# Optimization experiments

Measured on AMD Instinct MI355X. Metric: run time of the kernel, lower is better.

## Reference

```python
import jax, jax.numpy as jnp
import numpy as np

# Fixed tetrahedral (kanchor=4) rotation->anchor permutation table, taken verbatim
# from the docstring in the original source (trace_idx_ori).
TRACE_IDX_ORI = jnp.array([
    [0, 1, 2, 3], [0, 2, 3, 1], [0, 3, 1, 2],
    [1, 2, 0, 3], [1, 0, 3, 2], [1, 3, 2, 0],
    [2, 3, 0, 1], [2, 0, 1, 3], [2, 1, 3, 0],
    [3, 1, 0, 2], [3, 0, 2, 1], [3, 2, 1, 0]], dtype=jnp.int32)

B, A, N, M, D, H = 1, 4, 384, 384, 256, 8
C = D // H  # d_model_per_head = 32
NR = TRACE_IDX_ORI.shape[0]  # 12 rotations


def _project_heads(x, W, b):
    # x: (b, a, n, d) -> (b, a, h, n, c)
    y = x @ W.T + b
    bb, aa, nn, _ = y.shape
    return y.reshape(bb, aa, nn, H, C).transpose(0, 1, 3, 2, 4)


def setup_inputs() -> dict:
    key = jax.random.key(0)
    ks = jax.random.split(key, 6)
    s = 1.0 / np.sqrt(D).astype(np.float32)
    return {
        "input_q": jax.random.normal(ks[0], (B, A, N, D), dtype=jnp.float32),
        "input_k": jax.random.normal(ks[1], (B, A, M, D), dtype=jnp.float32),
        "input_v": jax.random.normal(ks[2], (B, A, M, D), dtype=jnp.float32),
        "Wq": jax.random.normal(ks[3], (D, D), dtype=jnp.float32) * s,
        "bq": jnp.zeros((D,), dtype=jnp.float32),
        "Wk": jax.random.normal(ks[4], (D, D), dtype=jnp.float32) * s,
        "bk": jnp.zeros((D,), dtype=jnp.float32),
        "Wv": jax.random.normal(ks[5], (D, D), dtype=jnp.float32) * s,
        "bv": jnp.zeros((D,), dtype=jnp.float32),
    }


def reference(input_q, input_k, input_v, Wq, bq, Wk, bk, Wv, bv):
    # Step 0: linear projections + split heads.  q,k,v: (b, a, h, n|m, c)
    q = _project_heads(input_q, Wq, bq)
    k = _project_heads(input_k, Wk, bk)
    v = _project_heads(input_v, Wv, bv)

    # Step 1: per-anchor-pair local attention scores: (b, a, e, h, n, m)
    scores_ae = jnp.einsum('bahnc,behmc->baehnm', q, k) / jnp.sqrt(
        jnp.asarray(C, dtype=q.dtype))

    # Step 2: rotation-wise gather (attn_mode='r_soft', alternative_impl=False).
    # For rotation r, query anchor a attends to key anchor trace_idx_ori[r, a]:
    # scores_rot[b, r, a] = scores_ae[b, a, trace_idx_ori[r, a]]  -> (b, nr, a, h, n, m)
    a_idx = jnp.arange(A, dtype=jnp.int32)[None, :]  # (1, A) broadcasts vs (NR, A)
    scores_rot = scores_ae[:, a_idx, TRACE_IDX_ORI]

    # Global rotation attention: pool over anchors/heads/points (attn_r_summ='mean',
    # attn_r_multihead=False), make non-negative ('sq'), normalize over rotations.
    pooled = jnp.mean(scores_rot, axis=(2, 3, 4, 5))  # (b, nr)
    pos = pooled * pooled
    attn_r = pos / jnp.sum(pos, axis=-1, keepdims=True)  # (b, nr)

    # Step 3+4: softmax over key points per rotation, gather values per rotation,
    # then weight by the global rotation attention.
    attn_local = jax.nn.softmax(scores_rot, axis=-1)  # (b, nr, a, h, n, m)
    v_rot = v[:, TRACE_IDX_ORI]  # (b, nr, a, h, m, c)
    hidden = jnp.einsum('br,brahnm,brahmc->bahnc', attn_r, attn_local, v_rot)

    # Merge heads: (b, a, h, n, c) -> (b, a, n, h*c)
    out = hidden.transpose(0, 1, 3, 2, 4).reshape(B, A, N, D)
    return out
```

## Files before the change

### kernel.cpp

```cpp
#include <hip/hip_runtime.h>
#include <hip/hip_bf16.h>

typedef __attribute__((ext_vector_type(8))) short s8x8;
typedef __attribute__((ext_vector_type(4))) float f32x4;

union FragU { s8x8 v; unsigned d[4]; };

__device__ __forceinline__ ushort f2bf(float x) {
    union { float f; unsigned u; } c; c.f = x;
    unsigned r = c.u + 0x7FFFu + ((c.u >> 16) & 1u);
    return (ushort)(r >> 16);
}
__device__ __forceinline__ float bf2f(ushort b) {
    union { unsigned u; float f; } c; c.u = ((unsigned)b) << 16;
    return c.f;
}
__device__ __forceinline__ unsigned cvt_pk(float lo, float hi) {
    unsigned r;
    asm("v_cvt_pk_bf16_f32 %0, %1, %2" : "=v"(r) : "v"(lo), "v"(hi));
    return r;
}
__device__ __forceinline__ float asf(unsigned u) {
    union { unsigned u; float f; } c; c.u = u; return c.f;
}

__global__ __launch_bounds__(64) void proj_kernel(
    const float* __restrict__ Xq, const float* __restrict__ Xk,
    const float* __restrict__ Xv,
    const float* __restrict__ Wq, const float* __restrict__ bq,
    const float* __restrict__ Wk, const float* __restrict__ bk,
    const float* __restrict__ Wv, const float* __restrict__ bv,
    ushort* __restrict__ qh, ushort* __restrict__ ql,
    ushort* __restrict__ kh, ushort* __restrict__ kl,
    ushort* __restrict__ vh, float* __restrict__ part)
{
    const int z = blockIdx.z;
    const float* X    = (z == 0) ? Xq : (z == 1) ? Xk : Xv;
    const float* W    = (z == 0) ? Wq : (z == 1) ? Wk : Wv;
    const float* bias = (z == 0) ? bq : (z == 1) ? bk : bv;

    const int lane = threadIdx.x;
    const int lg   = lane >> 4;
    const int ll   = lane & 15;
    const int bx   = blockIdx.x;
    const int row0 = bx * 16;
    const int col0 = blockIdx.y * 64;

    f32x4 acc[4];
    #pragma unroll
    for (int ct = 0; ct < 4; ++ct) acc[ct] = (f32x4){0.f, 0.f, 0.f, 0.f};

    for (int kk = 0; kk < 8; ++kk) {
        FragU ah, al;
        {
            const float* xp = &X[(size_t)(row0 + ll) * 256 + kk * 32 + lg * 8];
            const float4 x0 = *(const float4*)&xp[0];
            const float4 x1 = *(const float4*)&xp[4];
            const float xv[8] = {x0.x, x0.y, x0.z, x0.w, x1.x, x1.y, x1.z, x1.w};
            #pragma unroll
            for (int i = 0; i < 4; ++i) {
                const unsigned hd = cvt_pk(xv[2 * i], xv[2 * i + 1]);
                ah.d[i] = hd;
                al.d[i] = cvt_pk(xv[2 * i]     - asf(hd << 16),
                                 xv[2 * i + 1] - asf(hd & 0xffff0000u));
            }
        }
        #pragma unroll
        for (int ct = 0; ct < 4; ++ct) {
            const float* wp = &W[(size_t)(col0 + ct * 16 + ll) * 256 + kk * 32 + lg * 8];
            const float4 w0 = *(const float4*)&wp[0];
            const float4 w1 = *(const float4*)&wp[4];
            const float wv[8] = {w0.x, w0.y, w0.z, w0.w, w1.x, w1.y, w1.z, w1.w};
            FragU bh, bl;
            #pragma unroll
            for (int i = 0; i < 4; ++i) {
                const unsigned hd = cvt_pk(wv[2 * i], wv[2 * i + 1]);
                bh.d[i] = hd;
                bl.d[i] = cvt_pk(wv[2 * i]     - asf(hd << 16),
                                 wv[2 * i + 1] - asf(hd & 0xffff0000u));
            }
            acc[ct] = __builtin_amdgcn_mfma_f32_16x16x32_bf16(ah.v, bh.v, acc[ct], 0, 0, 0);
            acc[ct] = __builtin_amdgcn_mfma_f32_16x16x32_bf16(al.v, bh.v, acc[ct], 0, 0, 0);
            acc[ct] = __builtin_amdgcn_mfma_f32_16x16x32_bf16(ah.v, bl.v, acc[ct], 0, 0, 0);
        }
    }

    const int ae  = bx / 24;
    const int rbl = bx - ae * 24;
    float bct[4];
    #pragma unroll
    for (int ct = 0; ct < 4; ++ct) bct[ct] = bias[col0 + ct * 16 + ll];

    if (z != 2) {
        #pragma unroll
        for (int ct = 0; ct < 4; ++ct) {
            const int d = col0 + ct * 16 + ll;
            const int hd = d >> 5;
            const int c = d & 31;
            #pragma unroll
            for (int j = 0; j < 4; ++j) {
                const int n = rbl * 16 + lg * 4 + j;
                const float v = acc[ct][j] + bct[ct];
                const ushort hb = f2bf(v);
                const ushort lb = f2bf(v - bf2f(hb));
                if (z == 0) {
                    const size_t idx = ((size_t)((ae * 8 + hd) * 384 + n)) * 32 + c;
                    qh[idx] = hb; ql[idx] = lb;
                } else {
                    const size_t idx =
                        ((size_t)(((ae * 8 + hd) * 4 + (c >> 3)) * 384 + n)) * 8 + (c & 7);
                    kh[idx] = hb; kl[idx] = lb;
                }
            }
        }
        #pragma unroll
        for (int ct = 0; ct < 4; ++ct) {
            float cs = 4.f * bct[ct];
            #pragma unroll
            for (int j = 0; j < 4; ++j) cs += acc[ct][j];
            cs += __shfl_xor(cs, 16);
            cs += __shfl_xor(cs, 32);
            if (lg == 0)
                part[((size_t)(z * 4 + ae) * 24 + rbl) * 256 + col0 + ct * 16 + ll] = cs;
        }
    } else {
        #pragma unroll
        for (int ct = 0; ct < 4; ++ct) {
            const int d = col0 + ct * 16 + ll;
            const int hd = d >> 5;
            const int c = d & 31;
            ushort p[4];
            #pragma unroll
            for (int j = 0; j < 4; ++j) p[j] = f2bf(acc[ct][j] + bct[ct]);
            const int m0 = rbl * 16 + lg * 4;
            const size_t basei = ((size_t)((ae * 8 + hd) * 32 + c)) * 384 + m0;
            *(uint2*)&vh[basei] =
                make_uint2((unsigned)p[0] | ((unsigned)p[1] << 16),
                           (unsigned)p[2] | ((unsigned)p[3] << 16));
        }
    }
}

__global__ __launch_bounds__(256) void stats_kernel(
    const float* __restrict__ part, float* __restrict__ wout)
{
    __shared__ float ws4[4][16];
    __shared__ float cellsh[16];
    const int tid = threadIdx.x;
    const int lane = tid & 63;
    const int wv = tid >> 6;

    float qs[4], ks[4];
    #pragma unroll
    for (int a2 = 0; a2 < 4; ++a2) {
        const float* pq = &part[(size_t)(0 * 4 + a2) * 24 * 256 + tid];
        const float* pk = &part[(size_t)(1 * 4 + a2) * 24 * 256 + tid];
        float sq = 0.f, sk = 0.f;
        #pragma unroll
        for (int r = 0; r < 24; ++r) {
            sq += pq[r * 256];
            sk += pk[r * 256];
        }
        qs[a2] = sq; ks[a2] = sk;
    }
    #pragma unroll
    for (int i = 0; i < 16; ++i) {
        float v = qs[i >> 2] * ks[i & 3];
        v += __shfl_xor(v, 1);
        v += __shfl_xor(v, 2);
        v += __shfl_xor(v, 4);
        v += __shfl_xor(v, 8);
        v += __shfl_xor(v, 16);
        v += __shfl_xor(v, 32);
        if (lane == 0) ws4[wv][i] = v;
    }
    __syncthreads();
    if (tid < 16)
        cellsh[tid] = 0.17677669529663687f *
            (ws4[0][tid] + ws4[1][tid] + ws4[2][tid] + ws4[3][tid]);
    __syncthreads();
    if (tid == 0) {
        const int TR[12][4] = {
            {0,1,2,3},{0,2,3,1},{0,3,1,2},{1,2,0,3},{1,0,3,2},{1,3,2,0},
            {2,3,0,1},{2,0,1,3},{2,1,3,0},{3,1,0,2},{3,0,2,1},{3,2,1,0}};
        const float denom = 4.0f * 8.0f * 384.0f * 384.0f;
        float pos[12];
        float psum = 0.f;
        for (int r = 0; r < 12; ++r) {
            float s = 0.f;
            for (int a2 = 0; a2 < 4; ++a2) s += cellsh[a2 * 4 + TR[r][a2]];
            const float pooled = s / denom;
            pos[r] = pooled * pooled;
            psum += pos[r];
        }
        float w[16];
        for (int i = 0; i < 16; ++i) w[i] = 0.f;
        const float ip = 1.f / psum;
        for (int r = 0; r < 12; ++r)
            for (int a2 = 0; a2 < 4; ++a2) w[a2 * 4 + TR[r][a2]] += pos[r] * ip;
        for (int i = 0; i < 16; ++i) wout[i] = w[i];
    }
}

__global__ __launch_bounds__(192) void attn_mfma_kernel(
    const ushort* __restrict__ qhb, const ushort* __restrict__ qlb,
    const ushort* __restrict__ khb, const ushort* __restrict__ klb,
    const ushort* __restrict__ vhb, float* __restrict__ Sout)
{
    __shared__ ushort Kh[4 * 1544];
    __shared__ ushort Kl[4 * 1544];
    __shared__ ushort Vh[32 * 200];
    __shared__ ushort Pl[3 * 2 * 16 * 40];

    const int strip = blockIdx.x;
    const int aeh   = blockIdx.y;
    const int hh    = aeh & 7;
    const int ee    = (aeh >> 3) & 3;
    const int aa    = aeh >> 5;
    const int e8h   = ee * 8 + hh;
    const int a8h   = aa * 8 + hh;
    const int tid   = threadIdx.x;
    const int wave  = tid >> 6;
    const int lane  = tid & 63;
    const int lg    = lane >> 4;
    const int ll    = lane & 15;

    s8x8 qfh[2], qfl[2];
    #pragma unroll
    for (int r = 0; r < 2; ++r) {
        const int n0 = strip * 96 + (2 * wave + r) * 16;
        const size_t off = (size_t)(a8h * 384 + n0 + ll) * 32 + lg * 8;
        qfh[r] = *(const s8x8*)&qhb[off];
        qfl[r] = *(const s8x8*)&qlb[off];
    }

    f32x4 oacc[2][2];
    #pragma unroll
    for (int r = 0; r < 2; ++r)
        #pragma unroll
        for (int ct = 0; ct < 2; ++ct)
            oacc[r][ct] = (f32x4){0.f, 0.f, 0.f, 0.f};
    float lsum[2][4];
    #pragma unroll
    for (int r = 0; r < 2; ++r)
        #pragma unroll
        for (int j = 0; j < 4; ++j) lsum[r][j] = 0.f;
    const float sc = 0.17677669529663687f;

    for (int half = 0; half < 2; ++half) {
        #pragma unroll
        for (int i = 0; i < 4; ++i) {
            const size_t src = ((size_t)(e8h * 4 + i) * 384 + half * 192 + tid) * 8;
            *(uint4*)&Kh[i * 1544 + tid * 8] = *(const uint4*)&khb[src];
            *(uint4*)&Kl[i * 1544 + tid * 8] = *(const uint4*)&klb[src];
        }
        #pragma unroll
        for (int i = 0; i < 4; ++i) {
            const int u = tid + 192 * i;
            const int c = u / 24;
            const int m8 = (u - c * 24) * 8;
            *(uint4*)&Vh[c * 200 + m8] =
                *(const uint4*)&vhb[(size_t)(e8h * 32 + c) * 384 + half * 192 + m8];
        }
        __syncthreads();

        for (int mt2 = 0; mt2 < 6; ++mt2) {
            #pragma unroll
            for (int sub = 0; sub < 2; ++sub) {
                const int mt = mt2 * 2 + sub;
                const s8x8 kfh = *(const s8x8*)&Kh[lg * 1544 + (mt * 16 + ll) * 8];
                const s8x8 kfl = *(const s8x8*)&Kl[lg * 1544 + (mt * 16 + ll) * 8];
                #pragma unroll
                for (int r = 0; r < 2; ++r) {
                    f32x4 s = {0.f, 0.f, 0.f, 0.f};
                    __builtin_amdgcn_s_setprio(1);
                    s = __builtin_amdgcn_mfma_f32_16x16x32_bf16(qfh[r], kfh, s, 0, 0, 0);
                    s = __builtin_amdgcn_mfma_f32_16x16x32_bf16(qfl[r], kfh, s, 0, 0, 0);
                    s = __builtin_amdgcn_mfma_f32_16x16x32_bf16(qfh[r], kfl, s, 0, 0, 0);
                    __builtin_amdgcn_s_setprio(0);
                    #pragma unroll
                    for (int j = 0; j < 4; ++j) {
                        const float p = __expf(s[j] * sc);
                        lsum[r][j] += p;
                        Pl[((wave * 2 + r) * 16 + lg * 4 + j) * 40 + sub * 16 + ll] = f2bf(p);
                    }
                }
            }
            const int mloc = mt2 * 32;
            const s8x8 vf0 = *(const s8x8*)&Vh[(0  + ll) * 200 + mloc + lg * 8];
            const s8x8 vf1 = *(const s8x8*)&Vh[(16 + ll) * 200 + mloc + lg * 8];
            #pragma unroll
            for (int r = 0; r < 2; ++r) {
                const s8x8 pa = *(const s8x8*)&Pl[((wave * 2 + r) * 16 + ll) * 40 + lg * 8];
                __builtin_amdgcn_s_setprio(1);
                oacc[r][0] = __builtin_amdgcn_mfma_f32_16x16x32_bf16(pa, vf0, oacc[r][0], 0, 0, 0);
                oacc[r][1] = __builtin_amdgcn_mfma_f32_16x16x32_bf16(pa, vf1, oacc[r][1], 0, 0, 0);
                __builtin_amdgcn_s_setprio(0);
            }
        }
        __syncthreads();
    }

    #pragma unroll
    for (int r = 0; r < 2; ++r) {
        #pragma unroll
        for (int j = 0; j < 4; ++j) {
            float L = lsum[r][j];
            L += __shfl_xor(L, 1);
            L += __shfl_xor(L, 2);
            L += __shfl_xor(L, 4);
            L += __shfl_xor(L, 8);
            const float invL = 1.f / L;
            const int row = strip * 96 + (2 * wave + r) * 16 + lg * 4 + j;
            const size_t base = (size_t)(aeh * 384 + row) * 32;
            Sout[base + 0  + ll] = oacc[r][0][j] * invL;
            Sout[base + 16 + ll] = oacc[r][1][j] * invL;
        }
    }
}

__global__ __launch_bounds__(256) void combine_kernel(
    const float* __restrict__ S, const float* __restrict__ wbuf,
    float* __restrict__ out)
{
    __shared__ float wsh[16];
    const int tid = threadIdx.x;
    if (tid < 16) wsh[tid] = wbuf[tid];
    __syncthreads();

    const int idx4 = blockIdx.x * 256 + tid;
    const int a = idx4 / 24576;
    const int rem = idx4 - a * 24576;
    const int n = rem >> 6;
    const int d4 = rem & 63;
    const int h = d4 >> 3;
    const int c0 = (d4 & 7) * 4;
    float4 r = make_float4(0.f, 0.f, 0.f, 0.f);
    #pragma unroll
    for (int e = 0; e < 4; ++e) {
        const float wv2 = wsh[a * 4 + e];
        const float4 s = *(const float4*)&S[(size_t)(((a * 4 + e) * 8 + h) * 384 + n) * 32 + c0];
        r.x += wv2 * s.x; r.y += wv2 * s.y; r.z += wv2 * s.z; r.w += wv2 * s.w;
    }
    *(float4*)&out[(size_t)idx4 * 4] = r;
}

extern "C" void kernel_launch(void* const* d_in, const int* in_sizes, int n_in,
                              void* d_out, int out_size, void* d_ws, size_t ws_size,
                              hipStream_t stream)
{
    const float* in_q = (const float*)d_in[0];
    const float* in_k = (const float*)d_in[1];
    const float* in_v = (const float*)d_in[2];
    const float* Wq   = (const float*)d_in[3];
    const float* bq   = (const float*)d_in[4];
    const float* Wk   = (const float*)d_in[5];
    const float* bk   = (const float*)d_in[6];
    const float* Wv   = (const float*)d_in[7];
    const float* bv   = (const float*)d_in[8];

    ushort* qh = (ushort*)d_ws;
    ushort* ql = qh + 393216;
    ushort* kh = ql + 393216;
    ushort* kl = kh + 393216;
    ushort* vh = kl + 393216;
    float*  Sb = (float*)(vh + 393216);
    float*  pt = Sb + 1572864;
    float*  wb = pt + 49152;
    float*  outp = (float*)d_out;

    dim3 pgrid(96, 4, 3);
    proj_kernel<<<pgrid, 64, 0, stream>>>(in_q, in_k, in_v, Wq, bq, Wk, bk,
                                          Wv, bv, qh, ql, kh, kl, vh, pt);
    stats_kernel<<<1, 256, 0, stream>>>(pt, wb);
    dim3 agrid(4, 128);
    attn_mfma_kernel<<<agrid, 192, 0, stream>>>(qh, ql, kh, kl, vh, Sb);
    combine_kernel<<<384, 256, 0, stream>>>(Sb, wb, outp);
}
```

Before: 47.31 us.

## Fuse rotation-weighted combine into attention kernel, loop over key anchors in-block

The attention kernel now owns one (anchor, head) pair and a 48-row query strip, and loops over all four key anchors inside the block. It weights each anchor's normalized output by the rotation weight and accumulates in registers, then writes the final merged-head output directly. This removes the fp32 intermediate buffer S and the separate combine kernel launch, along with their global write and read traffic. In exchange each wave holds one query tile instead of two, so K/V shared-memory tiles get less reuse per load. The grid is also smaller (256 blocks instead of 512), with a longer serial loop per block.

```diff
diff --git a/kernel.cpp b/kernel.cpp
--- a/kernel.cpp
+++ b/kernel.cpp
@@ -202,147 +202,116 @@
     }
 }
 
-__global__ __launch_bounds__(192) void attn_mfma_kernel(
+__global__ __launch_bounds__(192) void attn_fused_kernel(
     const ushort* __restrict__ qhb, const ushort* __restrict__ qlb,
     const ushort* __restrict__ khb, const ushort* __restrict__ klb,
-    const ushort* __restrict__ vhb, float* __restrict__ Sout)
+    const ushort* __restrict__ vhb, const float* __restrict__ wbuf,
+    float* __restrict__ out)
 {
     __shared__ ushort Kh[4 * 1544];
     __shared__ ushort Kl[4 * 1544];
     __shared__ ushort Vh[32 * 200];
-    __shared__ ushort Pl[3 * 2 * 16 * 40];
+    __shared__ ushort Pl[48 * 40];
 
     const int strip = blockIdx.x;
-    const int aeh   = blockIdx.y;
-    const int hh    = aeh & 7;
-    const int ee    = (aeh >> 3) & 3;
-    const int aa    = aeh >> 5;
-    const int e8h   = ee * 8 + hh;
-    const int a8h   = aa * 8 + hh;
+    const int ah    = blockIdx.y;
+    const int hh    = ah & 7;
+    const int aa    = ah >> 3;
     const int tid   = threadIdx.x;
     const int wave  = tid >> 6;
     const int lane  = tid & 63;
     const int lg    = lane >> 4;
     const int ll    = lane & 15;
 
-    s8x8 qfh[2], qfl[2];
-    #pragma unroll
-    for (int r = 0; r < 2; ++r) {
-        const int n0 = strip * 96 + (2 * wave + r) * 16;
-        const size_t off = (size_t)(a8h * 384 + n0 + ll) * 32 + lg * 8;
-        qfh[r] = *(const s8x8*)&qhb[off];
-        qfl[r] = *(const s8x8*)&qlb[off];
-    }
-
-    f32x4 oacc[2][2];
-    #pragma unroll
-    for (int r = 0; r < 2; ++r)
-        #pragma unroll
-        for (int ct = 0; ct < 2; ++ct)
-            oacc[r][ct] = (f32x4){0.f, 0.f, 0.f, 0.f};
-    float lsum[2][4];
-    #pragma unroll
-    for (int r = 0; r < 2; ++r)
-        #pragma unroll
-        for (int j = 0; j < 4; ++j) lsum[r][j] = 0.f;
+    const int n0 = strip * 48 + wave * 16;
+    s8x8 qfh, qfl;
+    {
+        const size_t off = (size_t)(ah * 384 + n0 + ll) * 32 + lg * 8;
+        qfh = *(const s8x8*)&qhb[off];
+        qfl = *(const s8x8*)&qlb[off];
+    }
+
+    f32x4 oout[2];
+    oout[0] = (f32x4){0.f, 0.f, 0.f, 0.f};
+    oout[1] = (f32x4){0.f, 0.f, 0.f, 0.f};
     const float sc = 0.17677669529663687f;
 
-    for (int half = 0; half < 2; ++half) {
-        #pragma unroll
-        for (int i = 0; i < 4; ++i) {
-            const size_t src = ((size_t)(e8h * 4 + i) * 384 + half * 192 + tid) * 8;
-            *(uint4*)&Kh[i * 1544 + tid * 8] = *(const uint4*)&khb[src];
-            *(uint4*)&Kl[i * 1544 + tid * 8] = *(const uint4*)&klb[src];
-        }
-        #pragma unroll
-        for (int i = 0; i < 4; ++i) {
-            const int u = tid + 192 * i;
-            const int c = u / 24;
-            const int m8 = (u - c * 24) * 8;
-            *(uint4*)&Vh[c * 200 + m8] =
-                *(const uint4*)&vhb[(size_t)(e8h * 32 + c) * 384 + half * 192 + m8];
-        }
-        __syncthreads();
-
-        for (int mt2 = 0; mt2 < 6; ++mt2) {
-            #pragma unroll
-            for (int sub = 0; sub < 2; ++sub) {
-                const int mt = mt2 * 2 + sub;
-                const s8x8 kfh = *(const s8x8*)&Kh[lg * 1544 + (mt * 16 + ll) * 8];
-                const s8x8 kfl = *(const s8x8*)&Kl[lg * 1544 + (mt * 16 + ll) * 8];
+    for (int e = 0; e < 4; ++e) {
+        const int e8h = e * 8 + hh;
+        f32x4 oacc[2];
+        oacc[0] = (f32x4){0.f, 0.f, 0.f, 0.f};
+        oacc[1] = (f32x4){0.f, 0.f, 0.f, 0.f};
+        float lsum[4] = {0.f, 0.f, 0.f, 0.f};
+
+        for (int half = 0; half < 2; ++half) {
+            #pragma unroll
+            for (int i = 0; i < 4; ++i) {
+                const size_t src = ((size_t)(e8h * 4 + i) * 384 + half * 192 + tid) * 8;
+                *(uint4*)&Kh[i * 1544 + tid * 8] = *(const uint4*)&khb[src];
+                *(uint4*)&Kl[i * 1544 + tid * 8] = *(const uint4*)&klb[src];
+            }
+            #pragma unroll
+            for (int i = 0; i < 4; ++i) {
+                const int u = tid + 192 * i;
+                const int c = u / 24;
+                const int m8 = (u - c * 24) * 8;
+                *(uint4*)&Vh[c * 200 + m8] =
+                    *(const uint4*)&vhb[(size_t)(e8h * 32 + c) * 384 + half * 192 + m8];
+            }
+            __syncthreads();
+
+            for (int mt2 = 0; mt2 < 6; ++mt2) {
                 #pragma unroll
-                for (int r = 0; r < 2; ++r) {
+                for (int sub = 0; sub < 2; ++sub) {
+                    const int mt = mt2 * 2 + sub;
+                    const s8x8 kfh = *(const s8x8*)&Kh[lg * 1544 + (mt * 16 + ll) * 8];
+                    const s8x8 kfl = *(const s8x8*)&Kl[lg * 1544 + (mt * 16 + ll) * 8];
                     f32x4 s = {0.f, 0.f, 0.f, 0.f};
                     __builtin_amdgcn_s_setprio(1);
-                    s = __builtin_amdgcn_mfma_f32_16x16x32_bf16(qfh[r], kfh, s, 0, 0, 0);
-                    s = __builtin_amdgcn_mfma_f32_16x16x32_bf16(qfl[r], kfh, s, 0, 0, 0);
-                    s = __builtin_amdgcn_mfma_f32_16x16x32_bf16(qfh[r], kfl, s, 0, 0, 0);
+                    s = __builtin_amdgcn_mfma_f32_16x16x32_bf16(qfh, kfh, s, 0, 0, 0);
+                    s = __builtin_amdgcn_mfma_f32_16x16x32_bf16(qfl, kfh, s, 0, 0, 0);
+                    s = __builtin_amdgcn_mfma_f32_16x16x32_bf16(qfh, kfl, s, 0, 0, 0);
                     __builtin_amdgcn_s_setprio(0);
                     #pragma unroll
                     for (int j = 0; j < 4; ++j) {
                         const float p = __expf(s[j] * sc);
-                        lsum[r][j] += p;
-                        Pl[((wave * 2 + r) * 16 + lg * 4 + j) * 40 + sub * 16 + ll] = f2bf(p);
+                        lsum[j] += p;
+                        Pl[(wave * 16 + lg * 4 + j) * 40 + sub * 16 + ll] = f2bf(p);
                     }
                 }
-            }
-            const int mloc = mt2 * 32;
-            const s8x8 vf0 = *(const s8x8*)&Vh[(0  + ll) * 200 + mloc + lg * 8];
-            const s8x8 vf1 = *(const s8x8*)&Vh[(16 + ll) * 200 + mloc + lg * 8];
-            #pragma unroll
-            for (int r = 0; r < 2; ++r) {
-                const s8x8 pa = *(const s8x8*)&Pl[((wave * 2 + r) * 16 + ll) * 40 + lg * 8];
+                const int mloc = mt2 * 32;
+                const s8x8 vf0 = *(const s8x8*)&Vh[(0  + ll) * 200 + mloc + lg * 8];
+                const s8x8 vf1 = *(const s8x8*)&Vh[(16 + ll) * 200 + mloc + lg * 8];
+                const s8x8 pa = *(const s8x8*)&Pl[(wave * 16 + ll) * 40 + lg * 8];
                 __builtin_amdgcn_s_setprio(1);
-                oacc[r][0] = __builtin_amdgcn_mfma_f32_16x16x32_bf16(pa, vf0, oacc[r][0], 0, 0, 0);
-                oacc[r][1] = __builtin_amdgcn_mfma_f32_16x16x32_bf16(pa, vf1, oacc[r][1], 0, 0, 0);
+                oacc[0] = __builtin_amdgcn_mfma_f32_16x16x32_bf16(pa, vf0, oacc[0], 0, 0, 0);
+                oacc[1] = __builtin_amdgcn_mfma_f32_16x16x32_bf16(pa, vf1, oacc[1], 0, 0, 0);
                 __builtin_amdgcn_s_setprio(0);
             }
-        }
-        __syncthreads();
-    }
-
-    #pragma unroll
-    for (int r = 0; r < 2; ++r) {
+            __syncthreads();
+        }
+
+        const float we = wbuf[aa * 4 + e];
         #pragma unroll
         for (int j = 0; j < 4; ++j) {
-            float L = lsum[r][j];
+            float L = lsum[j];
             L += __shfl_xor(L, 1);
             L += __shfl_xor(L, 2);
             L += __shfl_xor(L, 4);
             L += __shfl_xor(L, 8);
-            const float invL = 1.f / L;
-            const int row = strip * 96 + (2 * wave + r) * 16 + lg * 4 + j;
-            const size_t base = (size_t)(aeh * 384 + row) * 32;
-            Sout[base + 0  + ll] = oacc[r][0][j] * invL;
-            Sout[base + 16 + ll] = oacc[r][1][j] * invL;
-        }
-    }
-}
-
-__global__ __launch_bounds__(256) void combine_kernel(
-    const float* __restrict__ S, const float* __restrict__ wbuf,
-    float* __restrict__ out)
-{
-    __shared__ float wsh[16];
-    const int tid = threadIdx.x;
-    if (tid < 16) wsh[tid] = wbuf[tid];
-    __syncthreads();
-
-    const int idx4 = blockIdx.x * 256 + tid;
-    const int a = idx4 / 24576;
-    const int rem = idx4 - a * 24576;
-    const int n = rem >> 6;
-    const int d4 = rem & 63;
-    const int h = d4 >> 3;
-    const int c0 = (d4 & 7) * 4;
-    float4 r = make_float4(0.f, 0.f, 0.f, 0.f);
-    #pragma unroll
-    for (int e = 0; e < 4; ++e) {
-        const float wv2 = wsh[a * 4 + e];
-        const float4 s = *(const float4*)&S[(size_t)(((a * 4 + e) * 8 + h) * 384 + n) * 32 + c0];
-        r.x += wv2 * s.x; r.y += wv2 * s.y; r.z += wv2 * s.z; r.w += wv2 * s.w;
-    }
-    *(float4*)&out[(size_t)idx4 * 4] = r;
+            const float f = we / L;
+            oout[0][j] += f * oacc[0][j];
+            oout[1][j] += f * oacc[1][j];
+        }
+    }
+
+    #pragma unroll
+    for (int j = 0; j < 4; ++j) {
+        const int row = n0 + lg * 4 + j;
+        const size_t base = ((size_t)(aa * 384 + row)) * 256 + hh * 32;
+        out[base + 0  + ll] = oout[0][j];
+        out[base + 16 + ll] = oout[1][j];
+    }
 }
 
 extern "C" void kernel_launch(void* const* d_in, const int* in_sizes, int n_in,
@@ -364,8 +333,7 @@
     ushort* kh = ql + 393216;
     ushort* kl = kh + 393216;
     ushort* vh = kl + 393216;
-    float*  Sb = (float*)(vh + 393216);
-    float*  pt = Sb + 1572864;
+    float*  pt = (float*)(vh + 393216);
     float*  wb = pt + 49152;
     float*  outp = (float*)d_out;
 
@@ -373,7 +341,6 @@
     proj_kernel<<<pgrid, 64, 0, stream>>>(in_q, in_k, in_v, Wq, bq, Wk, bk,
                                           Wv, bv, qh, ql, kh, kl, vh, pt);
     stats_kernel<<<1, 256, 0, stream>>>(pt, wb);
-    dim3 agrid(4, 128);
-    attn_mfma_kernel<<<agrid, 192, 0, stream>>>(qh, ql, kh, kl, vh, Sb);
-    combine_kernel<<<384, 256, 0, stream>>>(Sb, wb, outp);
-}
+    dim3 agrid(8, 32);
+    attn_fused_kernel<<<agrid, 192, 0, stream>>>(qh, ql, kh, kl, vh, wb, outp);
+}
```

New measurement: 53.97 us. 14.1% more time.

## Keep softmax probabilities in registers via transposed QK MFMA; pack projection waves

Applied to the files above, without the earlier changes.

The attention kernel swaps the QK^T MFMA operand order so each lane holds score values that already match the A-operand layout of the PV MFMA. The probabilities are packed to bf16 in registers instead of going through a shared-memory round trip, and the V tile is stored to LDS with a permuted column order to match. The row-sum reduction changes from per-element sums with a 4-step shuffle to per-lane accumulation followed by cross-group shuffles and a broadcast. Separately, the projection kernel now packs three 64-thread tasks into each 192-thread block, cutting the block count.

```diff
diff --git a/kernel.cpp b/kernel.cpp
--- a/kernel.cpp
+++ b/kernel.cpp
@@ -24,7 +24,7 @@
     union { unsigned u; float f; } c; c.u = u; return c.f;
 }
 
-__global__ __launch_bounds__(64) void proj_kernel(
+__global__ __launch_bounds__(192) void proj_kernel(
     const float* __restrict__ Xq, const float* __restrict__ Xk,
     const float* __restrict__ Xv,
     const float* __restrict__ Wq, const float* __restrict__ bq,
@@ -34,17 +34,23 @@
     ushort* __restrict__ kh, ushort* __restrict__ kl,
     ushort* __restrict__ vh, float* __restrict__ part)
 {
-    const int z = blockIdx.z;
+    const int tid  = threadIdx.x;
+    const int wave = tid >> 6;
+    const int lane = tid & 63;
+    const int task = blockIdx.x * 3 + wave;
+    const int z    = task / 384;
+    const int rem  = task - z * 384;
+    const int by   = rem / 96;
+    const int bx   = rem - by * 96;
+
     const float* X    = (z == 0) ? Xq : (z == 1) ? Xk : Xv;
     const float* W    = (z == 0) ? Wq : (z == 1) ? Wk : Wv;
     const float* bias = (z == 0) ? bq : (z == 1) ? bk : bv;
 
-    const int lane = threadIdx.x;
     const int lg   = lane >> 4;
     const int ll   = lane & 15;
-    const int bx   = blockIdx.x;
     const int row0 = bx * 16;
-    const int col0 = blockIdx.y * 64;
+    const int col0 = by * 64;
 
     f32x4 acc[4];
     #pragma unroll
@@ -210,7 +216,6 @@
     __shared__ ushort Kh[4 * 1544];
     __shared__ ushort Kl[4 * 1544];
     __shared__ ushort Vh[32 * 200];
-    __shared__ ushort Pl[3 * 2 * 16 * 40];
 
     const int strip = blockIdx.x;
     const int aeh   = blockIdx.y;
@@ -240,11 +245,7 @@
         #pragma unroll
         for (int ct = 0; ct < 2; ++ct)
             oacc[r][ct] = (f32x4){0.f, 0.f, 0.f, 0.f};
-    float lsum[2][4];
-    #pragma unroll
-    for (int r = 0; r < 2; ++r)
-        #pragma unroll
-        for (int j = 0; j < 4; ++j) lsum[r][j] = 0.f;
+    float lsum[2] = {0.f, 0.f};
     const float sc = 0.17677669529663687f;
 
     for (int half = 0; half < 2; ++half) {
@@ -258,13 +259,19 @@
         for (int i = 0; i < 4; ++i) {
             const int u = tid + 192 * i;
             const int c = u / 24;
-            const int m8 = (u - c * 24) * 8;
-            *(uint4*)&Vh[c * 200 + m8] =
-                *(const uint4*)&vhb[(size_t)(e8h * 32 + c) * 384 + half * 192 + m8];
+            const int t = u - c * 24;
+            const int M = (t >> 2) * 32;
+            const int q2 = t & 3;
+            const int off = (q2 & 1) * 16 + (q2 >> 1) * 4;
+            const uint4 src = *(const uint4*)
+                &vhb[(size_t)(e8h * 32 + c) * 384 + half * 192 + t * 8];
+            *(uint2*)&Vh[c * 200 + M + off]     = make_uint2(src.x, src.y);
+            *(uint2*)&Vh[c * 200 + M + off + 8] = make_uint2(src.z, src.w);
         }
         __syncthreads();
 
         for (int mt2 = 0; mt2 < 6; ++mt2) {
+            float pv_[2][8];
             #pragma unroll
             for (int sub = 0; sub < 2; ++sub) {
                 const int mt = mt2 * 2 + sub;
@@ -274,15 +281,15 @@
                 for (int r = 0; r < 2; ++r) {
                     f32x4 s = {0.f, 0.f, 0.f, 0.f};
                     __builtin_amdgcn_s_setprio(1);
-                    s = __builtin_amdgcn_mfma_f32_16x16x32_bf16(qfh[r], kfh, s, 0, 0, 0);
-                    s = __builtin_amdgcn_mfma_f32_16x16x32_bf16(qfl[r], kfh, s, 0, 0, 0);
-                    s = __builtin_amdgcn_mfma_f32_16x16x32_bf16(qfh[r], kfl, s, 0, 0, 0);
+                    s = __builtin_amdgcn_mfma_f32_16x16x32_bf16(kfh, qfh[r], s, 0, 0, 0);
+                    s = __builtin_amdgcn_mfma_f32_16x16x32_bf16(kfl, qfh[r], s, 0, 0, 0);
+                    s = __builtin_amdgcn_mfma_f32_16x16x32_bf16(kfh, qfl[r], s, 0, 0, 0);
                     __builtin_amdgcn_s_setprio(0);
                     #pragma unroll
                     for (int j = 0; j < 4; ++j) {
                         const float p = __expf(s[j] * sc);
-                        lsum[r][j] += p;
-                        Pl[((wave * 2 + r) * 16 + lg * 4 + j) * 40 + sub * 16 + ll] = f2bf(p);
+                        lsum[r] += p;
+                        pv_[r][sub * 4 + j] = p;
                     }
                 }
             }
@@ -291,10 +298,14 @@
             const s8x8 vf1 = *(const s8x8*)&Vh[(16 + ll) * 200 + mloc + lg * 8];
             #pragma unroll
             for (int r = 0; r < 2; ++r) {
-                const s8x8 pa = *(const s8x8*)&Pl[((wave * 2 + r) * 16 + ll) * 40 + lg * 8];
+                FragU pu;
+                pu.d[0] = cvt_pk(pv_[r][0], pv_[r][1]);
+                pu.d[1] = cvt_pk(pv_[r][2], pv_[r][3]);
+                pu.d[2] = cvt_pk(pv_[r][4], pv_[r][5]);
+                pu.d[3] = cvt_pk(pv_[r][6], pv_[r][7]);
                 __builtin_amdgcn_s_setprio(1);
-                oacc[r][0] = __builtin_amdgcn_mfma_f32_16x16x32_bf16(pa, vf0, oacc[r][0], 0, 0, 0);
-                oacc[r][1] = __builtin_amdgcn_mfma_f32_16x16x32_bf16(pa, vf1, oacc[r][1], 0, 0, 0);
+                oacc[r][0] = __builtin_amdgcn_mfma_f32_16x16x32_bf16(pu.v, vf0, oacc[r][0], 0, 0, 0);
+                oacc[r][1] = __builtin_amdgcn_mfma_f32_16x16x32_bf16(pu.v, vf1, oacc[r][1], 0, 0, 0);
                 __builtin_amdgcn_s_setprio(0);
             }
         }
@@ -303,14 +314,13 @@
 
     #pragma unroll
     for (int r = 0; r < 2; ++r) {
+        float L = lsum[r];
+        L += __shfl_xor(L, 16);
+        L += __shfl_xor(L, 32);
         #pragma unroll
         for (int j = 0; j < 4; ++j) {
-            float L = lsum[r][j];
-            L += __shfl_xor(L, 1);
-            L += __shfl_xor(L, 2);
-            L += __shfl_xor(L, 4);
-            L += __shfl_xor(L, 8);
-            const float invL = 1.f / L;
+            const float Lrow = __shfl(L, lg * 4 + j);
+            const float invL = 1.f / Lrow;
             const int row = strip * 96 + (2 * wave + r) * 16 + lg * 4 + j;
             const size_t base = (size_t)(aeh * 384 + row) * 32;
             Sout[base + 0  + ll] = oacc[r][0][j] * invL;
@@ -369,9 +379,8 @@
     float*  wb = pt + 49152;
     float*  outp = (float*)d_out;
 
-    dim3 pgrid(96, 4, 3);
-    proj_kernel<<<pgrid, 64, 0, stream>>>(in_q, in_k, in_v, Wq, bq, Wk, bk,
-                                          Wv, bv, qh, ql, kh, kl, vh, pt);
+    proj_kernel<<<384, 192, 0, stream>>>(in_q, in_k, in_v, Wq, bq, Wk, bk,
+                                         Wv, bv, qh, ql, kh, kl, vh, pt);
     stats_kernel<<<1, 256, 0, stream>>>(pt, wb);
     dim3 agrid(4, 128);
     attn_mfma_kernel<<<agrid, 192, 0, stream>>>(qh, ql, kh, kl, vh, Sb);
```

Result: faster. 46.01 us (-2.7%).
